# Kernel tuning notes

Hardware: AMD Instinct MI355X
Metric: run time of the kernel (lower is better)

The kernel has to match this reference:

```python
import jax, jax.numpy as jnp
import numpy as np

EPS = 1e-12
TOPK = 6

def _l2norm(x):
    # matches torch F.normalize(p=2, eps=1e-12)
    n = jnp.linalg.norm(x, axis=-1, keepdims=True)
    return x / jnp.maximum(n, EPS)

def setup_inputs() -> dict:
    key = jax.random.key(0)
    k1, k2 = jax.random.split(key)
    nC, M, P, d = 5, 512, 196, 384
    support = jax.random.normal(k1, (nC, P, d), dtype=jnp.float32)
    query = jax.random.normal(k2, (M, P, d), dtype=jnp.float32)
    scale_cls = jnp.full((1,), 10.0, dtype=jnp.float32)  # init value in module
    bias = jnp.zeros((1,), dtype=jnp.float32)
    return {"support": support, "query": query, "scale_cls": scale_cls, "bias": bias}

def reference(support, query, scale_cls, bias):
    q = _l2norm(query)      # [M, P, d]
    s = _l2norm(support)    # [nC, P, d]
    # batched cosine similarity between every query patch and support patch
    sim = jnp.einsum('mpd,cqd->mcpq', q, s)   # [M, nC, P, P]
    # max over support patches, then sum of top-6 query-patch matches
    m = sim.max(axis=3)                        # [M, nC, P]
    top6 = jax.lax.top_k(m, TOPK)[0].sum(axis=-1)  # [M, nC]
    cls_scores = top6[None]                    # [1, M, nC] (unsqueeze(0))
    return scale_cls * (cls_scores + bias)
```

## Files before the change

### kernel.cpp

```cpp
#include <hip/hip_runtime.h>
#include <hip/hip_bf16.h>
#include <cstdint>

typedef __attribute__((ext_vector_type(8))) short short8;
typedef __attribute__((ext_vector_type(4))) float floatx4;

#define NC   5
#define PP   196
#define DD   384
#define MM   512
#define ROWS (MM * PP)
#define NRB  1568
#define EPSN 1e-12f

#define NTILES      16
#define TILE_BYTES  49152
#define KSTEP_BYTES 4096

__device__ __forceinline__ unsigned enc_f(float f) {
    unsigned u = __float_as_uint(f);
    return (u & 0x80000000u) ? ~u : (u | 0x80000000u);
}
__device__ __forceinline__ float dec_f(unsigned u) {
    unsigned b = (u & 0x80000000u) ? (u ^ 0x80000000u) : ~u;
    return __uint_as_float(b);
}
#define ENC_NEG_INF 0x007FFFFFu

__device__ __forceinline__ int cls_of(int col) {
    return (col >= 784) ? 4 : (col >= 588) ? 3 : (col >= 392) ? 2 : (col >= 196) ? 1 : 0;
}

__global__ __launch_bounds__(256) void k_norm0(const float* __restrict__ sup,
                                               float* __restrict__ sinv) {
    int wid = threadIdx.x >> 6, lane = threadIdx.x & 63;
    int r = blockIdx.x * 4 + wid;
    if (r >= NC * PP) return;
    const float* src = sup + (size_t)r * DD;
    float s = 0.f;
    #pragma unroll
    for (int j = 0; j < 6; ++j) { float v = src[lane + j * 64]; s += v * v; }
    #pragma unroll
    for (int off = 1; off < 64; off <<= 1) s += __shfl_xor(s, off, 64);
    if (lane == 0) sinv[r] = 1.0f / fmaxf(sqrtf(s), EPSN);
}

__global__ __launch_bounds__(256) void k_swz(const float* __restrict__ sup,
                                             const float* __restrict__ sinv,
                                             __hip_bfloat16* __restrict__ snw) {
    int s = blockIdx.x * 256 + threadIdx.x;
    int lane = s & 63;
    int r1 = s >> 6;
    int ct = r1 & 3;
    int r2 = r1 >> 2;
    int kk = r2 % 12;
    int t  = r2 / 12;
    int c16 = lane & 15, quad = lane >> 4;
    int col = t * 64 + ct * 16 + c16;
    if (col > NC * PP - 1) col = NC * PP - 1;
    int srow = col;
    const float* sp = sup + (size_t)srow * DD + kk * 32 + quad * 8;
    float inv = sinv[srow];
    alignas(16) __hip_bfloat16 hb[8];
    #pragma unroll
    for (int e = 0; e < 8; ++e) hb[e] = __float2bfloat16(sp[e] * inv);
    *(uint4*)((char*)snw + (size_t)s * 16) = *(const uint4*)hb;
}

__global__ __launch_bounds__(256, 3) void k_gemm_max(const float* __restrict__ q,
                                                     const __hip_bfloat16* __restrict__ snw,
                                                     float* __restrict__ rowmaxg) {
    __shared__ __hip_bfloat16 As[12 * 4 * 64 * 8];
    __shared__ unsigned rmax[64 * NC];
    __shared__ float rss[64];

    const int tid  = threadIdx.x;
    const int row0 = blockIdx.x * 64;
    const int lane = tid & 63;
    const int wav  = tid >> 6;

    for (int i = tid; i < 64 * NC; i += 256) rmax[i] = ENC_NEG_INF;

    {
        const int arow = tid >> 2;
        const int asub = tid & 3;
        const int rt   = arow >> 4, c16 = arow & 15;
        const float* src = q + (size_t)(row0 + arow) * DD;
        float ss = 0.f;
        #pragma unroll
        for (int i = 0; i < 12; ++i) {
            int ch = asub + i * 4;
            const floatx4* p = (const floatx4*)(src + ch * 8);
            floatx4 x0 = __builtin_nontemporal_load(p);
            floatx4 x1 = __builtin_nontemporal_load(p + 1);
            ss += x0.x*x0.x + x0.y*x0.y + x0.z*x0.z + x0.w*x0.w
                + x1.x*x1.x + x1.y*x1.y + x1.z*x1.z + x1.w*x1.w;
            alignas(16) __hip_bfloat16 hb[8];
            hb[0] = __float2bfloat16(x0.x); hb[1] = __float2bfloat16(x0.y);
            hb[2] = __float2bfloat16(x0.z); hb[3] = __float2bfloat16(x0.w);
            hb[4] = __float2bfloat16(x1.x); hb[5] = __float2bfloat16(x1.y);
            hb[6] = __float2bfloat16(x1.z); hb[7] = __float2bfloat16(x1.w);
            int kk = ch >> 2, quad = ch & 3;
            *(uint4*)&As[(((kk * 4 + rt) * 64) + quad * 16 + c16) * 8] = *(const uint4*)hb;
        }
        ss += __shfl_xor(ss, 1, 64);
        ss += __shfl_xor(ss, 2, 64);
        if (asub == 0) rss[arow] = ss;
    }

    const char* bbase = (const char*)snw + (size_t)wav * TILE_BYTES + (size_t)lane * 16;
    short8 b0[4], b1[4], b2[4], a[4];
    #pragma unroll
    for (int ct = 0; ct < 4; ++ct) b0[ct] = ((const short8*)(bbase + 0 * KSTEP_BYTES))[ct * 64];
    #pragma unroll
    for (int ct = 0; ct < 4; ++ct) b1[ct] = ((const short8*)(bbase + 1 * KSTEP_BYTES))[ct * 64];
    #pragma unroll
    for (int ct = 0; ct < 4; ++ct) b2[ct] = ((const short8*)(bbase + 2 * KSTEP_BYTES))[ct * 64];

    __syncthreads();

    #define LOAD_NEXT(buf, step)                                                     \
        do {                                                                         \
            int nk = kk + 3 + (step);                                                \
            if (nk < 12) {                                                           \
                _Pragma("unroll")                                                    \
                for (int ct = 0; ct < 4; ++ct)                                       \
                    buf[ct] = ((const short8*)(bbase + nk * KSTEP_BYTES))[ct * 64];  \
            } else if (g + 4 < NTILES) {                                             \
                _Pragma("unroll")                                                    \
                for (int ct = 0; ct < 4; ++ct)                                       \
                    buf[ct] = ((const short8*)(bbase + 4 * TILE_BYTES +              \
                                               (nk - 12) * KSTEP_BYTES))[ct * 64];   \
            }                                                                        \
        } while (0)

    #define MFMA_STEP(buf, kkoff)                                                    \
        do {                                                                         \
            _Pragma("unroll")                                                        \
            for (int rt = 0; rt < 4; ++rt)                                           \
                a[rt] = *(const short8*)&As[(((kk + (kkoff)) * 4 + rt) * 64 + lane) * 8]; \
            _Pragma("unroll")                                                        \
            for (int rt = 0; rt < 4; ++rt)                                           \
                _Pragma("unroll")                                                    \
                for (int ct = 0; ct < 4; ++ct)                                       \
                    acc[rt][ct] = __builtin_amdgcn_mfma_f32_16x16x32_bf16(           \
                        a[rt], buf[ct], acc[rt][ct], 0, 0, 0);                       \
        } while (0)

    #pragma unroll 1
    for (int g = wav; g < NTILES; g += 4) {
        floatx4 acc[4][4];
        #pragma unroll
        for (int i = 0; i < 4; ++i)
            #pragma unroll
            for (int j = 0; j < 4; ++j) acc[i][j] = (floatx4){0.f, 0.f, 0.f, 0.f};

        #pragma unroll 1
        for (int kk = 0; kk < 12; kk += 3) {
            MFMA_STEP(b0, 0); LOAD_NEXT(b0, 0);
            MFMA_STEP(b1, 1); LOAD_NEXT(b1, 1);
            MFMA_STEP(b2, 2); LOAD_NEXT(b2, 2);
        }

        {
            const int colbase = g * 64;
            int ce = colbase + 63; if (ce > NC * PP - 1) ce = NC * PP - 1;
            const int clo = cls_of(colbase), chi = cls_of(ce);
            const int quad = lane >> 4, c16 = lane & 15;
            if (clo == chi) {
                #pragma unroll
                for (int rt = 0; rt < 4; ++rt) {
                    #pragma unroll
                    for (int reg = 0; reg < 4; ++reg) {
                        float mx = fmaxf(fmaxf(acc[rt][0][reg], acc[rt][1][reg]),
                                         fmaxf(acc[rt][2][reg], acc[rt][3][reg]));
                        #pragma unroll
                        for (int off = 1; off < 16; off <<= 1)
                            mx = fmaxf(mx, __shfl_xor(mx, off, 64));
                        if (c16 == 0) {
                            int rloc = rt * 16 + quad * 4 + reg;
                            atomicMax(&rmax[rloc * NC + clo], enc_f(mx));
                        }
                    }
                }
            } else {
                int lcls[4];
                #pragma unroll
                for (int ct = 0; ct < 4; ++ct) {
                    int col = colbase + ct * 16 + c16;
                    if (col > NC * PP - 1) col = NC * PP - 1;
                    lcls[ct] = cls_of(col);
                }
                #pragma unroll 1
                for (int cc = clo; cc <= chi; ++cc) {
                    #pragma unroll
                    for (int rt = 0; rt < 4; ++rt) {
                        #pragma unroll
                        for (int reg = 0; reg < 4; ++reg) {
                            float mx = -INFINITY;
                            #pragma unroll
                            for (int ct = 0; ct < 4; ++ct)
                                if (lcls[ct] == cc) mx = fmaxf(mx, acc[rt][ct][reg]);
                            #pragma unroll
                            for (int off = 1; off < 16; off <<= 1)
                                mx = fmaxf(mx, __shfl_xor(mx, off, 64));
                            if (c16 == 0) {
                                int rloc = rt * 16 + quad * 4 + reg;
                                atomicMax(&rmax[rloc * NC + cc], enc_f(mx));
                            }
                        }
                    }
                }
            }
        }
        bbase += 4 * TILE_BYTES;
    }

    __syncthreads();
    for (int i = tid; i < 64 * NC; i += 256) {
        int c = i >> 6, row = i & 63;
        float inv = 1.0f / fmaxf(sqrtf(rss[row]), EPSN);
        __builtin_nontemporal_store(dec_f(rmax[row * NC + c]) * inv,
                                    &rowmaxg[(size_t)c * ROWS + row0 + row]);
    }
}

__global__ __launch_bounds__(256) void k_top6(const float* __restrict__ rowmaxg,
                                              const float* __restrict__ scale,
                                              const float* __restrict__ bias,
                                              float* __restrict__ out) {
    int wav = threadIdx.x >> 6, lane = threadIdx.x & 63;
    int pair = blockIdx.x * 4 + wav;
    if (pair >= MM * NC) return;
    int m = pair / NC, c = pair % NC;
    size_t base = (size_t)c * ROWS + (size_t)m * PP;
    float v[4];
    #pragma unroll
    for (int i = 0; i < 4; ++i) {
        int p = lane + i * 64;
        v[i] = (p < PP) ? rowmaxg[base + p] : -INFINITY;
    }
    float sum = 0.f;
    for (int t = 0; t < 6; ++t) {
        float bv = v[0]; int bi = 0;
        #pragma unroll
        for (int i = 1; i < 4; ++i) { if (v[i] > bv) { bv = v[i]; bi = i; } }
        int gid = bi * 64 + lane;
        #pragma unroll
        for (int off = 1; off < 64; off <<= 1) {
            float ov = __shfl_xor(bv, off, 64);
            int og  = __shfl_xor(gid, off, 64);
            if (ov > bv || (ov == bv && og < gid)) { bv = ov; gid = og; }
        }
        sum += bv;
        if ((gid & 63) == lane) v[gid >> 6] = -INFINITY;
    }
    if (lane == 0) out[pair] = scale[0] * (sum + bias[0]);
}

extern "C" void kernel_launch(void* const* d_in, const int* in_sizes, int n_in,
                              void* d_out, int out_size, void* d_ws, size_t ws_size,
                              hipStream_t stream) {
    const float* support = (const float*)d_in[0];
    const float* query   = (const float*)d_in[1];
    const float* scale   = (const float*)d_in[2];
    const float* bias    = (const float*)d_in[3];
    float* out = (float*)d_out;

    char* ws = (char*)d_ws;
    __hip_bfloat16* snw = (__hip_bfloat16*)ws;
    float* sinv         = (float*)(ws + 786432);
    float* rowmaxg      = (float*)(ws + 786432 + 4096);

    hipLaunchKernelGGL(k_norm0,   dim3(245),  dim3(256), 0, stream, support, sinv);
    hipLaunchKernelGGL(k_swz,     dim3(192),  dim3(256), 0, stream, support, sinv, snw);
    hipLaunchKernelGGL(k_gemm_max,dim3(NRB),  dim3(256), 0, stream, query, snw, rowmaxg);
    hipLaunchKernelGGL(k_top6,    dim3(640),  dim3(256), 0, stream, rowmaxg, scale, bias, out);
}
```

Measured before the change: 312.8 us.

## Halve query rows per block and swap MFMA operands to simplify max reduction

Measured after the change: 304.5 us. 2.6% less time.

```diff
diff --git a/kernel.cpp b/kernel.cpp
--- a/kernel.cpp
+++ b/kernel.cpp
@@ -10,7 +10,8 @@
 #define DD   384
 #define MM   512
 #define ROWS (MM * PP)
-#define NRB  1568
+#define NRB  3136
+#define BR   32
 #define EPSN 1e-12f
 
 #define NTILES      16
@@ -67,29 +68,29 @@
     *(uint4*)((char*)snw + (size_t)s * 16) = *(const uint4*)hb;
 }
 
-__global__ __launch_bounds__(256, 3) void k_gemm_max(const float* __restrict__ q,
+__global__ __launch_bounds__(256, 4) void k_gemm_max(const float* __restrict__ q,
                                                      const __hip_bfloat16* __restrict__ snw,
                                                      float* __restrict__ rowmaxg) {
-    __shared__ __hip_bfloat16 As[12 * 4 * 64 * 8];
-    __shared__ unsigned rmax[64 * NC];
-    __shared__ float rss[64];
+    __shared__ __hip_bfloat16 As[12 * 2 * 64 * 8];
+    __shared__ unsigned rmax[BR * NC];
+    __shared__ float rss[BR];
 
     const int tid  = threadIdx.x;
-    const int row0 = blockIdx.x * 64;
+    const int row0 = blockIdx.x * BR;
     const int lane = tid & 63;
     const int wav  = tid >> 6;
 
-    for (int i = tid; i < 64 * NC; i += 256) rmax[i] = ENC_NEG_INF;
+    for (int i = tid; i < BR * NC; i += 256) rmax[i] = ENC_NEG_INF;
 
     {
-        const int arow = tid >> 2;
-        const int asub = tid & 3;
+        const int arow = tid >> 3;
+        const int asub = tid & 7;
         const int rt   = arow >> 4, c16 = arow & 15;
         const float* src = q + (size_t)(row0 + arow) * DD;
         float ss = 0.f;
         #pragma unroll
-        for (int i = 0; i < 12; ++i) {
-            int ch = asub + i * 4;
+        for (int i = 0; i < 6; ++i) {
+            int ch = asub + i * 8;
             const floatx4* p = (const floatx4*)(src + ch * 8);
             floatx4 x0 = __builtin_nontemporal_load(p);
             floatx4 x1 = __builtin_nontemporal_load(p + 1);
@@ -101,15 +102,16 @@
             hb[4] = __float2bfloat16(x1.x); hb[5] = __float2bfloat16(x1.y);
             hb[6] = __float2bfloat16(x1.z); hb[7] = __float2bfloat16(x1.w);
             int kk = ch >> 2, quad = ch & 3;
-            *(uint4*)&As[(((kk * 4 + rt) * 64) + quad * 16 + c16) * 8] = *(const uint4*)hb;
+            *(uint4*)&As[((kk * 2 + rt) * 64 + quad * 16 + c16) * 8] = *(const uint4*)hb;
         }
         ss += __shfl_xor(ss, 1, 64);
         ss += __shfl_xor(ss, 2, 64);
+        ss += __shfl_xor(ss, 4, 64);
         if (asub == 0) rss[arow] = ss;
     }
 
     const char* bbase = (const char*)snw + (size_t)wav * TILE_BYTES + (size_t)lane * 16;
-    short8 b0[4], b1[4], b2[4], a[4];
+    short8 b0[4], b1[4], b2[4], a[2];
     #pragma unroll
     for (int ct = 0; ct < 4; ++ct) b0[ct] = ((const short8*)(bbase + 0 * KSTEP_BYTES))[ct * 64];
     #pragma unroll
@@ -137,23 +139,23 @@
     #define MFMA_STEP(buf, kkoff)                                                    \
         do {                                                                         \
             _Pragma("unroll")                                                        \
-            for (int rt = 0; rt < 4; ++rt)                                           \
-                a[rt] = *(const short8*)&As[(((kk + (kkoff)) * 4 + rt) * 64 + lane) * 8]; \
+            for (int rt = 0; rt < 2; ++rt)                                           \
+                a[rt] = *(const short8*)&As[(((kk + (kkoff)) * 2 + rt) * 64 + lane) * 8]; \
             _Pragma("unroll")                                                        \
-            for (int rt = 0; rt < 4; ++rt)                                           \
+            for (int ct = 0; ct < 4; ++ct)                                           \
                 _Pragma("unroll")                                                    \
-                for (int ct = 0; ct < 4; ++ct)                                       \
-                    acc[rt][ct] = __builtin_amdgcn_mfma_f32_16x16x32_bf16(           \
-                        a[rt], buf[ct], acc[rt][ct], 0, 0, 0);                       \
+                for (int rt = 0; rt < 2; ++rt)                                       \
+                    acc[ct][rt] = __builtin_amdgcn_mfma_f32_16x16x32_bf16(           \
+                        buf[ct], a[rt], acc[ct][rt], 0, 0, 0);                       \
         } while (0)
 
     #pragma unroll 1
     for (int g = wav; g < NTILES; g += 4) {
-        floatx4 acc[4][4];
+        floatx4 acc[4][2];
         #pragma unroll
         for (int i = 0; i < 4; ++i)
             #pragma unroll
-            for (int j = 0; j < 4; ++j) acc[i][j] = (floatx4){0.f, 0.f, 0.f, 0.f};
+            for (int j = 0; j < 2; ++j) acc[i][j] = (floatx4){0.f, 0.f, 0.f, 0.f};
 
         #pragma unroll 1
         for (int kk = 0; kk < 12; kk += 3) {
@@ -166,49 +168,40 @@
             const int colbase = g * 64;
             int ce = colbase + 63; if (ce > NC * PP - 1) ce = NC * PP - 1;
             const int clo = cls_of(colbase), chi = cls_of(ce);
-            const int quad = lane >> 4, c16 = lane & 15;
+            const int quad = lane >> 4;
             if (clo == chi) {
                 #pragma unroll
-                for (int rt = 0; rt < 4; ++rt) {
+                for (int rt = 0; rt < 2; ++rt) {
+                    float mx = acc[0][rt][0];
                     #pragma unroll
-                    for (int reg = 0; reg < 4; ++reg) {
-                        float mx = fmaxf(fmaxf(acc[rt][0][reg], acc[rt][1][reg]),
-                                         fmaxf(acc[rt][2][reg], acc[rt][3][reg]));
+                    for (int ct = 0; ct < 4; ++ct)
                         #pragma unroll
-                        for (int off = 1; off < 16; off <<= 1)
-                            mx = fmaxf(mx, __shfl_xor(mx, off, 64));
-                        if (c16 == 0) {
-                            int rloc = rt * 16 + quad * 4 + reg;
-                            atomicMax(&rmax[rloc * NC + clo], enc_f(mx));
-                        }
-                    }
+                        for (int reg = 0; reg < 4; ++reg)
+                            if (ct | reg) mx = fmaxf(mx, acc[ct][rt][reg]);
+                    mx = fmaxf(mx, __shfl_xor(mx, 16, 64));
+                    mx = fmaxf(mx, __shfl_xor(mx, 32, 64));
+                    if (lane < 16) atomicMax(&rmax[(rt * 16 + lane) * NC + clo], enc_f(mx));
                 }
             } else {
-                int lcls[4];
+                const int bnd = chi * PP;
                 #pragma unroll
-                for (int ct = 0; ct < 4; ++ct) {
-                    int col = colbase + ct * 16 + c16;
-                    if (col > NC * PP - 1) col = NC * PP - 1;
-                    lcls[ct] = cls_of(col);
-                }
-                #pragma unroll 1
-                for (int cc = clo; cc <= chi; ++cc) {
+                for (int rt = 0; rt < 2; ++rt) {
+                    float mlo = -INFINITY, mhi = -INFINITY;
                     #pragma unroll
-                    for (int rt = 0; rt < 4; ++rt) {
+                    for (int ct = 0; ct < 4; ++ct)
                         #pragma unroll
                         for (int reg = 0; reg < 4; ++reg) {
-                            float mx = -INFINITY;
-                            #pragma unroll
-                            for (int ct = 0; ct < 4; ++ct)
-                                if (lcls[ct] == cc) mx = fmaxf(mx, acc[rt][ct][reg]);
-                            #pragma unroll
-                            for (int off = 1; off < 16; off <<= 1)
-                                mx = fmaxf(mx, __shfl_xor(mx, off, 64));
-                            if (c16 == 0) {
-                                int rloc = rt * 16 + quad * 4 + reg;
-                                atomicMax(&rmax[rloc * NC + cc], enc_f(mx));
-                            }
+                            int scol = colbase + ct * 16 + quad * 4 + reg;
+                            if (scol >= bnd) mhi = fmaxf(mhi, acc[ct][rt][reg]);
+                            else             mlo = fmaxf(mlo, acc[ct][rt][reg]);
                         }
+                    mlo = fmaxf(mlo, __shfl_xor(mlo, 16, 64));
+                    mlo = fmaxf(mlo, __shfl_xor(mlo, 32, 64));
+                    mhi = fmaxf(mhi, __shfl_xor(mhi, 16, 64));
+                    mhi = fmaxf(mhi, __shfl_xor(mhi, 32, 64));
+                    if (lane < 16) {
+                        atomicMax(&rmax[(rt * 16 + lane) * NC + clo], enc_f(mlo));
+                        atomicMax(&rmax[(rt * 16 + lane) * NC + chi], enc_f(mhi));
                     }
                 }
             }
@@ -217,8 +210,8 @@
     }
 
     __syncthreads();
-    for (int i = tid; i < 64 * NC; i += 256) {
-        int c = i >> 6, row = i & 63;
+    for (int i = tid; i < BR * NC; i += 256) {
+        int c = i >> 5, row = i & 31;
         float inv = 1.0f / fmaxf(sqrtf(rss[row]), EPSN);
         __builtin_nontemporal_store(dec_f(rmax[row * NC + c]) * inv,
                                     &rowmaxg[(size_t)c * ROWS + row0 + row]);
```
